# Optimization experiments

Measured on AMD Instinct MI355X. Metric: run time of the kernel, lower is better.

Reference implementation:

```python
import jax, jax.numpy as jnp
import numpy as np
from jax import lax

V, D = 100000, 300          # vocab, embedding dim (pretrained_embeds shape)
F, FS, K = 256, 3, 5        # nof_filters, filters_size, k_for_maxpool
B, NS, LS, LQ = 64, 50, 60, 32  # batch, n_sents per doc, sent len, question len


def setup_inputs() -> dict:
    key = jax.random.key(0)
    ks = jax.random.split(key, 8)
    sentences = jax.random.randint(ks[0], (B, NS, LS), 0, V)
    question = jax.random.randint(ks[1], (B, LQ), 0, V)
    target_sents = jax.random.randint(ks[2], (B, NS), 0, 2)
    target_docs = jax.random.randint(ks[3], (B,), 0, 2)
    embeds = jax.random.normal(ks[4], (V, D), dtype=jnp.float32)          # frozen pretrained table
    filters = jax.random.normal(ks[5], (F, 1, FS, D), dtype=jnp.float32)  # shared quest/sent conv filters
    W = jax.random.normal(ks[6], (6,), dtype=jnp.float32) * 0.4           # linear_per_q weight
    b = jax.random.normal(ks[7], (1,), dtype=jnp.float32) * 0.1           # linear_per_q bias
    return dict(sentences=sentences, question=question, target_sents=target_sents,
                target_docs=target_docs, embeds=embeds, filters=filters, W=W, b=b)


def _conv(x, filters):
    # x: [N,L,D], filters: [F,1,FS,D] -> [N,L,F]; matches F.conv2d(pad=(FS-1,0)) then slicing last L rows
    fs = filters.shape[2]
    L = x.shape[1]
    y = lax.conv_general_dilated(x[:, None, :, :], filters, (1, 1),
                                 ((fs - 1, fs - 1), (0, 0)),
                                 dimension_numbers=('NCHW', 'OIHW', 'NCHW'))  # [N,F,L+fs-1,1]
    return jnp.transpose(y[:, :, -L:, 0], (0, 2, 1))


def _cos(q, s):
    # q: [B,LQ,d], s: [B,NS,LS,d] -> [NS,B,LQ,LS] cosine similarity matrices
    num = jnp.einsum('bqd,bnld->nbql', q, s)
    qn = jnp.linalg.norm(q, axis=-1)                      # [B,LQ]
    sn = jnp.transpose(jnp.linalg.norm(s, axis=-1), (1, 0, 2))  # [NS,B,LS]
    return num / (qn[None, :, :, None] * sn[:, :, None, :])


def _pool(sim, k):
    # k-max pooling over the sentence-length axis -> stack [max, mean-of-top-k]
    top = lax.top_k(sim, k)[0]
    return jnp.stack([top[..., 0], jnp.mean(top, axis=-1)], axis=-1)


def _bce(p, t):
    eps = 1e-7
    p = jnp.clip(p, eps, 1.0 - eps)
    return -jnp.mean(t * jnp.log(p) + (1.0 - t) * jnp.log1p(-p))


def reference(sentences, question, target_sents, target_docs, embeds, filters, W, b):
    qe = embeds[question]                                 # [B,LQ,D]
    se = embeds[sentences]                                # [B,NS,LS,D]
    sim_ins = _cos(qe, se)                                # [NS,B,LQ,LS]
    sim_oh = (sim_ins >= 1.0 - 1e-5).astype(jnp.float32)  # exact-match channel (unmasked, as in original)
    qc = _conv(qe, filters)                               # [B,LQ,F]
    sc = _conv(se.reshape(B * NS, LS, D), filters).reshape(B, NS, LS, F)
    sim_sen = _cos(qc, sc)                                # [NS,B,LQ,LS]
    qmask = (question > 0).astype(jnp.float32)            # pad id = 0
    smask = (sentences > 0).astype(jnp.float32)
    m = qmask[None, :, :, None] * jnp.transpose(smask, (1, 0, 2))[:, :, None, :]
    feats = jnp.concatenate([_pool(sim_ins * m, K), _pool(sim_sen * m, K), _pool(sim_oh, K)], axis=-1)
    feats = jnp.transpose(feats, (1, 0, 2, 3))            # [B,NS,LQ,6]
    sent_out = jax.nn.sigmoid(feats @ W + b[0])           # [B,NS,LQ]
    sentence_relevance = jnp.mean(sent_out, axis=-1)      # [B,NS]
    document_emitions = jnp.max(sentence_relevance, axis=-1)  # [B]
    loss = (_bce(sentence_relevance, target_sents.astype(jnp.float32)) +
            _bce(document_emitions, target_docs.astype(jnp.float32))) / 2.0
    return loss, sentence_relevance, document_emitions
```

## Files before the change

### kernel.cpp

```cpp
#include <hip/hip_runtime.h>
#include <math.h>

#define VB  64
#define NSS 50
#define LSS 60
#define LQQ 32
#define DD  300
#define FF  256

#define SEST 312
#define SROWS 66
#define SCST 264
#define SIMST 66
#define KKC 29
#define KKI 10
#define KKS 8

typedef __attribute__((ext_vector_type(8))) short bfrag;
typedef __attribute__((ext_vector_type(4))) float ffrag;

__device__ __forceinline__ unsigned short f2bf(float v) {
    unsigned int x = __float_as_uint(v);
    x += 0x7fffu + ((x >> 16) & 1u);
    return (unsigned short)(x >> 16);
}
__device__ __forceinline__ float bf2f(unsigned short u) {
    return __uint_as_float(((unsigned int)u) << 16);
}

__global__ __launch_bounds__(256) void k_fprep(const float* __restrict__ filters,
                                               unsigned short* __restrict__ filt_frag) {
    int idx = blockIdx.x * 256 + threadIdx.x;
    const int total = KKC * 16 * 64 * 8;
    if (idx >= total) return;
    int j = idx & 7, ln = (idx >> 3) & 63, nt = (idx >> 9) & 15, kk = idx >> 13;
    int f = nt * 16 + (ln & 15);
    int k = kk * 32 + ((ln >> 4) << 3) + j;
    int t = k / SEST, d = k - t * SEST;
    unsigned short v = 0;
    if (t < 3 && d < DD) v = f2bf(filters[f * 900 + t * DD + d]);
    filt_frag[idx] = v;
}

__global__ __launch_bounds__(512) void k_qprep(const int* __restrict__ question,
                                               const float* __restrict__ embeds,
                                               const unsigned short* __restrict__ filt_frag,
                                               unsigned short* __restrict__ qe_frag,
                                               unsigned short* __restrict__ qc_frag,
                                               float* __restrict__ q_inv,
                                               float* __restrict__ qc_inv) {
    const int b = blockIdx.x, tid = threadIdx.x, lane = tid & 63, w = tid >> 6;
    const int quad = lane >> 4, m16 = lane & 15;
    __shared__ __align__(16) unsigned short qeb[34 * SEST];
    __shared__ __align__(16) unsigned short qcb[LQQ * SCST];
    const int* qrow = question + b * LQQ;
    {
        ushort4 z4 = {0, 0, 0, 0};
        for (int i = tid; i < 96; i += 512) {
            int r = i / 3, c = 300 + (i - r * 3) * 4;
            *(ushort4*)(qeb + r * SEST + c) = z4;
        }
        for (int i = tid; i < 156; i += 512) {
            int r = i / 78, c = (i - r * 78) * 4;
            *(ushort4*)(qeb + (LQQ + r) * SEST + c) = z4;
        }
    }
    for (int i = tid; i < LQQ * 75; i += 512) {
        int r = i / 75, c = (i - r * 75) * 4;
        float4 v = *(const float4*)(embeds + (size_t)qrow[r] * DD + c);
        ushort4 h;
        h.x = f2bf(v.x); h.y = f2bf(v.y); h.z = f2bf(v.z); h.w = f2bf(v.w);
        *(ushort4*)(qeb + r * SEST + c) = h;
    }
    __syncthreads();
    if (tid < 256) {
        int r = tid >> 3, part = tid & 7;
        float s = 0.f;
        #pragma unroll
        for (int it = 0; it < 5; ++it) {
            if (!(it == 4 && part == 7)) {
                int c = part * 8 + it * 64;
                uint4 u = *(const uint4*)(qeb + r * SEST + c);
                float a0 = bf2f((unsigned short)(u.x & 0xffff)), a1 = bf2f((unsigned short)(u.x >> 16));
                float a2 = bf2f((unsigned short)(u.y & 0xffff)), a3 = bf2f((unsigned short)(u.y >> 16));
                float a4 = bf2f((unsigned short)(u.z & 0xffff)), a5 = bf2f((unsigned short)(u.z >> 16));
                float a6 = bf2f((unsigned short)(u.w & 0xffff)), a7 = bf2f((unsigned short)(u.w >> 16));
                s += a0 * a0 + a1 * a1 + a2 * a2 + a3 * a3 + a4 * a4 + a5 * a5 + a6 * a6 + a7 * a7;
            }
        }
        s += __shfl_down(s, 4, 64);
        s += __shfl_down(s, 2, 64);
        s += __shfl_down(s, 1, 64);
        if (part == 0) q_inv[b * LQQ + r] = 1.f / sqrtf(s);
    }
    for (int idx = tid; idx < KKI * 2 * 512; idx += 512) {
        int j = idx & 7, ln = (idx >> 3) & 63, mt = (idx >> 9) & 1, kk = idx >> 10;
        int q = mt * 16 + (ln & 15);
        int k = kk * 32 + ((ln >> 4) << 3) + j;
        qe_frag[(size_t)b * (KKI * 2 * 512) + idx] = (k < DD) ? qeb[q * SEST + k] : (unsigned short)0;
    }
    const int mtq = w & 1, w4 = (w >> 1) * 4;
    ffrag acc[4];
    #pragma unroll
    for (int i = 0; i < 4; ++i) acc[i] = (ffrag)0.f;
    {
        const bfrag* fF = (const bfrag*)filt_frag;
        for (int kk = 0; kk < KKC; ++kk) {
            const int kb = kk * 32 + quad * 8;
            bfrag a0 = *(const bfrag*)(qeb + (mtq * 16 + m16) * SEST + kb);
            bfrag bb[4];
            #pragma unroll
            for (int i = 0; i < 4; ++i) bb[i] = fF[(kk * 16 + w4 + i) * 64 + lane];
            #pragma unroll
            for (int i = 0; i < 4; ++i)
                acc[i] = __builtin_amdgcn_mfma_f32_16x16x32_bf16(a0, bb[i], acc[i], 0, 0, 0);
        }
    }
    #pragma unroll
    for (int i = 0; i < 4; ++i) {
        int f = (w4 + i) * 16 + m16;
        #pragma unroll
        for (int r = 0; r < 4; ++r) {
            int q = mtq * 16 + quad * 4 + r;
            qcb[q * SCST + f] = f2bf(acc[i][r]);
        }
    }
    __syncthreads();
    if (tid < 256) {
        int r = tid >> 3, part = tid & 7;
        float s = 0.f;
        #pragma unroll
        for (int it = 0; it < 4; ++it) {
            int c = part * 8 + it * 64;
            uint4 u = *(const uint4*)(qcb + r * SCST + c);
            float a0 = bf2f((unsigned short)(u.x & 0xffff)), a1 = bf2f((unsigned short)(u.x >> 16));
            float a2 = bf2f((unsigned short)(u.y & 0xffff)), a3 = bf2f((unsigned short)(u.y >> 16));
            float a4 = bf2f((unsigned short)(u.z & 0xffff)), a5 = bf2f((unsigned short)(u.z >> 16));
            float a6 = bf2f((unsigned short)(u.w & 0xffff)), a7 = bf2f((unsigned short)(u.w >> 16));
            s += a0 * a0 + a1 * a1 + a2 * a2 + a3 * a3 + a4 * a4 + a5 * a5 + a6 * a6 + a7 * a7;
        }
        s += __shfl_down(s, 4, 64);
        s += __shfl_down(s, 2, 64);
        s += __shfl_down(s, 1, 64);
        if (part == 0) qc_inv[b * LQQ + r] = 1.f / sqrtf(s);
    }
    for (int idx = tid; idx < KKS * 2 * 512; idx += 512) {
        int j = idx & 7, ln = (idx >> 3) & 63, mt = (idx >> 9) & 1, kk = idx >> 10;
        int q = mt * 16 + (ln & 15);
        int k = kk * 32 + ((ln >> 4) << 3) + j;
        qc_frag[(size_t)b * (KKS * 2 * 512) + idx] = qcb[q * SCST + k];
    }
}

#define CONV_STEP(KKV, BB0, BB1) do {                                              \
    const int kb_ = (KKV) * 32 + quad * 8;                                         \
    bfrag a0_ = *(const bfrag*)(seb + (m16) * SEST + kb_);                         \
    bfrag a1_ = *(const bfrag*)(seb + (16 + m16) * SEST + kb_);                    \
    bfrag a2_ = *(const bfrag*)(seb + (32 + m16) * SEST + kb_);                    \
    bfrag a3_ = *(const bfrag*)(seb + (48 + m16) * SEST + kb_);                    \
    __builtin_amdgcn_s_setprio(1);                                                 \
    acc[0][0] = __builtin_amdgcn_mfma_f32_16x16x32_bf16(a0_, BB0, acc[0][0], 0, 0, 0); \
    acc[0][1] = __builtin_amdgcn_mfma_f32_16x16x32_bf16(a0_, BB1, acc[0][1], 0, 0, 0); \
    acc[1][0] = __builtin_amdgcn_mfma_f32_16x16x32_bf16(a1_, BB0, acc[1][0], 0, 0, 0); \
    acc[1][1] = __builtin_amdgcn_mfma_f32_16x16x32_bf16(a1_, BB1, acc[1][1], 0, 0, 0); \
    acc[2][0] = __builtin_amdgcn_mfma_f32_16x16x32_bf16(a2_, BB0, acc[2][0], 0, 0, 0); \
    acc[2][1] = __builtin_amdgcn_mfma_f32_16x16x32_bf16(a2_, BB1, acc[2][1], 0, 0, 0); \
    acc[3][0] = __builtin_amdgcn_mfma_f32_16x16x32_bf16(a3_, BB0, acc[3][0], 0, 0, 0); \
    acc[3][1] = __builtin_amdgcn_mfma_f32_16x16x32_bf16(a3_, BB1, acc[3][1], 0, 0, 0); \
    __builtin_amdgcn_s_setprio(0);                                                 \
} while (0)

__global__ __launch_bounds__(512, 6) void k_sent(
    const int* __restrict__ sentences, const int* __restrict__ question,
    const float* __restrict__ embeds,
    const unsigned short* __restrict__ filt_frag,
    const unsigned short* __restrict__ qe_frag,
    const unsigned short* __restrict__ qc_frag,
    const float* __restrict__ q_inv, const float* __restrict__ qc_inv,
    const float* __restrict__ W6, const float* __restrict__ b1,
    float* __restrict__ d_out) {
    const int blk = blockIdx.x;
    const int b = blk / NSS, n = blk - b * NSS;
    const int tid = threadIdx.x, lane = tid & 63, w = tid >> 6;
    const int quad = lane >> 4, m16 = lane & 15;
    const int w2 = w * 2;

    __shared__ __align__(16) unsigned short seb[SROWS * SEST];
    __shared__ __align__(16) float sim[LQQ * SIMST];
    __shared__ float sinv[64], scninv[64];
    __shared__ int sid[64];
    __shared__ int qid[LQQ];
    __shared__ float qm[LQQ], qiv[LQQ], qciv[LQQ];
    __shared__ float featq[LQQ][4];
    __shared__ float pr[LQQ];
    unsigned short* scb = seb;

    const bfrag* fF = (const bfrag*)filt_frag;
    bfrag b0a = fF[(w2) * 64 + lane];
    bfrag b0b = fF[(w2 + 1) * 64 + lane];

    const int* srow = sentences + ((size_t)b * NSS + n) * LSS;
    if (tid < 64) sid[tid] = (tid < LSS) ? srow[tid] : 0;
    if (tid < LQQ) {
        int qi = question[b * LQQ + tid];
        qid[tid] = qi; qm[tid] = qi > 0 ? 1.f : 0.f;
        qiv[tid] = q_inv[b * LQQ + tid]; qciv[tid] = qc_inv[b * LQQ + tid];
    }
    {
        ushort4 z4 = {0, 0, 0, 0};
        for (int i = tid; i < 180; i += 512) {
            int r = i / 3, c = 300 + (i - r * 3) * 4;
            *(ushort4*)(seb + r * SEST + c) = z4;
        }
        for (int i = tid; i < 468; i += 512) {
            int r = i / 78, c = (i - r * 78) * 4;
            *(ushort4*)(seb + (60 + r) * SEST + c) = z4;
        }
    }
    for (int i = tid; i < LSS * 75; i += 512) {
        int r = i / 75, c = (i - r * 75) * 4;
        float4 v = *(const float4*)(embeds + (size_t)srow[r] * DD + c);
        ushort4 h;
        h.x = f2bf(v.x); h.y = f2bf(v.y); h.z = f2bf(v.z); h.w = f2bf(v.w);
        *(ushort4*)(seb + r * SEST + c) = h;
    }
    __syncthreads();
    if (tid < 480) {
        int r = tid >> 3, part = tid & 7;
        float s = 0.f;
        #pragma unroll
        for (int it = 0; it < 5; ++it) {
            if (!(it == 4 && part == 7)) {
                int c = part * 8 + it * 64;
                uint4 u = *(const uint4*)(seb + r * SEST + c);
                float a0 = bf2f((unsigned short)(u.x & 0xffff)), a1 = bf2f((unsigned short)(u.x >> 16));
                float a2 = bf2f((unsigned short)(u.y & 0xffff)), a3 = bf2f((unsigned short)(u.y >> 16));
                float a4 = bf2f((unsigned short)(u.z & 0xffff)), a5 = bf2f((unsigned short)(u.z >> 16));
                float a6 = bf2f((unsigned short)(u.w & 0xffff)), a7 = bf2f((unsigned short)(u.w >> 16));
                s += a0 * a0 + a1 * a1 + a2 * a2 + a3 * a3 + a4 * a4 + a5 * a5 + a6 * a6 + a7 * a7;
            }
        }
        s += __shfl_down(s, 4, 64);
        s += __shfl_down(s, 2, 64);
        s += __shfl_down(s, 1, 64);
        if (part == 0) sinv[r] = 1.f / sqrtf(s);
    }
    if (tid >= 480 && tid < 484) sinv[60 + tid - 480] = 0.f;
    __syncthreads();

    ffrag acc[4][2];
    #pragma unroll
    for (int mt = 0; mt < 4; ++mt)
        #pragma unroll
        for (int i = 0; i < 2; ++i) acc[mt][i] = (ffrag)0.f;
    {
        bfrag b1a, b1b;
        for (int kk = 0; kk + 2 <= KKC; kk += 2) {
            b1a = fF[((kk + 1) * 16 + w2) * 64 + lane];
            b1b = fF[((kk + 1) * 16 + w2 + 1) * 64 + lane];
            CONV_STEP(kk, b0a, b0b);
            if (kk + 2 < KKC) {
                b0a = fF[((kk + 2) * 16 + w2) * 64 + lane];
                b0b = fF[((kk + 2) * 16 + w2 + 1) * 64 + lane];
            }
            CONV_STEP(kk + 1, b1a, b1b);
        }
        CONV_STEP(KKC - 1, b0a, b0b);
    }
    {
        const int mt = w >> 2, nt = w & 3;
        const bfrag* qF = (const bfrag*)qe_frag + ((size_t)b * KKI * 2 + mt) * 64 + lane;
        const unsigned short* sebr = seb + (nt * 16 + m16) * SEST + quad * 8;
        ffrag c0 = (ffrag)0.f;
        bfrag aq0 = qF[0];
        for (int kk = 0; kk < KKI; kk += 2) {
            bfrag aq1 = qF[(kk + 1) * 128];
            bfrag bL0 = *(const bfrag*)(sebr + kk * 32);
            c0 = __builtin_amdgcn_mfma_f32_16x16x32_bf16(aq0, bL0, c0, 0, 0, 0);
            if (kk + 2 < KKI) aq0 = qF[(kk + 2) * 128];
            bfrag bL1 = *(const bfrag*)(sebr + (kk + 1) * 32);
            c0 = __builtin_amdgcn_mfma_f32_16x16x32_bf16(aq1, bL1, c0, 0, 0, 0);
        }
        const int l_ = nt * 16 + m16;
        const float sm = sinv[l_] * (sid[l_] > 0 ? 1.f : 0.f);
        #pragma unroll
        for (int r = 0; r < 4; ++r) {
            int q = mt * 16 + quad * 4 + r;
            sim[q * SIMST + l_] = c0[r] * (qiv[q] * qm[q]) * sm;
        }
    }
    __syncthreads();

    if (tid < 256) {
        ushort4 z4 = {0, 0, 0, 0};
        int r4 = 60 + (tid >> 6), c4 = (tid & 63) * 4;
        *(ushort4*)(scb + r4 * SCST + c4) = z4;
    }
    #pragma unroll
    for (int mt = 0; mt < 4; ++mt)
        #pragma unroll
        for (int i = 0; i < 2; ++i) {
            int f = (w2 + i) * 16 + m16;
            #pragma unroll
            for (int r = 0; r < 4; ++r) {
                int l = mt * 16 + quad * 4 + r;
                scb[l * SCST + f] = f2bf(acc[mt][i][r]);
            }
        }
    if (tid < LQQ) {
        int q = tid;
        float t0 = -1e30f, t1 = -1e30f, t2 = -1e30f, t3 = -1e30f, t4 = -1e30f;
        for (int l = 0; l < LSS; ++l) {
            float v = sim[q * SIMST + l];
            if (v > t4) {
                if (v > t0)      { t4 = t3; t3 = t2; t2 = t1; t1 = t0; t0 = v; }
                else if (v > t1) { t4 = t3; t3 = t2; t2 = t1; t1 = v; }
                else if (v > t2) { t4 = t3; t3 = t2; t2 = v; }
                else if (v > t3) { t4 = t3; t3 = v; }
                else               t4 = v;
            }
        }
        featq[q][0] = t0;
        featq[q][1] = (t0 + t1 + t2 + t3 + t4) * 0.2f;
        int qi = qid[q], c = 0;
        for (int l = 0; l < LSS; ++l) c += (sid[l] == qi) ? 1 : 0;
        featq[q][2] = c > 0 ? 1.f : 0.f;
        featq[q][3] = (float)(c < 5 ? c : 5) * 0.2f;
    }
    __syncthreads();
    if (tid < 480) {
        int r = tid >> 3, part = tid & 7;
        float s = 0.f;
        #pragma unroll
        for (int it = 0; it < 4; ++it) {
            int c = part * 8 + it * 64;
            uint4 u = *(const uint4*)(scb + r * SCST + c);
            float a0 = bf2f((unsigned short)(u.x & 0xffff)), a1 = bf2f((unsigned short)(u.x >> 16));
            float a2 = bf2f((unsigned short)(u.y & 0xffff)), a3 = bf2f((unsigned short)(u.y >> 16));
            float a4 = bf2f((unsigned short)(u.z & 0xffff)), a5 = bf2f((unsigned short)(u.z >> 16));
            float a6 = bf2f((unsigned short)(u.w & 0xffff)), a7 = bf2f((unsigned short)(u.w >> 16));
            s += a0 * a0 + a1 * a1 + a2 * a2 + a3 * a3 + a4 * a4 + a5 * a5 + a6 * a6 + a7 * a7;
        }
        s += __shfl_down(s, 4, 64);
        s += __shfl_down(s, 2, 64);
        s += __shfl_down(s, 1, 64);
        if (part == 0) scninv[r] = 1.f / sqrtf(s);
    }
    if (tid >= 480 && tid < 484) scninv[60 + tid - 480] = 0.f;
    __syncthreads();
    {
        const int mt = w >> 2, nt = w & 3;
        const bfrag* qF = (const bfrag*)qc_frag + ((size_t)b * KKS * 2 + mt) * 64 + lane;
        const unsigned short* scbr = scb + (nt * 16 + m16) * SCST + quad * 8;
        ffrag c0 = (ffrag)0.f;
        bfrag aq0 = qF[0];
        for (int kk = 0; kk < KKS; kk += 2) {
            bfrag aq1 = qF[(kk + 1) * 128];
            bfrag bL0 = *(const bfrag*)(scbr + kk * 32);
            c0 = __builtin_amdgcn_mfma_f32_16x16x32_bf16(aq0, bL0, c0, 0, 0, 0);
            if (kk + 2 < KKS) aq0 = qF[(kk + 2) * 128];
            bfrag bL1 = *(const bfrag*)(scbr + (kk + 1) * 32);
            c0 = __builtin_amdgcn_mfma_f32_16x16x32_bf16(aq1, bL1, c0, 0, 0, 0);
        }
        const int l_ = nt * 16 + m16;
        const float sm = scninv[l_] * (sid[l_] > 0 ? 1.f : 0.f);
        #pragma unroll
        for (int r = 0; r < 4; ++r) {
            int q = mt * 16 + quad * 4 + r;
            sim[q * SIMST + l_] = c0[r] * (qciv[q] * qm[q]) * sm;
        }
    }
    __syncthreads();
    if (tid < LQQ) {
        int q = tid;
        float t0 = -1e30f, t1 = -1e30f, t2 = -1e30f, t3 = -1e30f, t4 = -1e30f;
        for (int l = 0; l < LSS; ++l) {
            float v = sim[q * SIMST + l];
            if (v > t4) {
                if (v > t0)      { t4 = t3; t3 = t2; t2 = t1; t1 = t0; t0 = v; }
                else if (v > t1) { t4 = t3; t3 = t2; t2 = t1; t1 = v; }
                else if (v > t2) { t4 = t3; t3 = t2; t2 = v; }
                else if (v > t3) { t4 = t3; t3 = v; }
                else               t4 = v;
            }
        }
        float smax = t0, smean = (t0 + t1 + t2 + t3 + t4) * 0.2f;
        float z = featq[q][0] * W6[0] + featq[q][1] * W6[1] + smax * W6[2] + smean * W6[3]
                + featq[q][2] * W6[4] + featq[q][3] * W6[5] + b1[0];
        pr[q] = 1.f / (1.f + expf(-z));
    }
    __syncthreads();
    if (w == 0) {
        float s = (lane < LQQ) ? pr[lane] : 0.f;
        s += __shfl_down(s, 16, 64);
        s += __shfl_down(s, 8, 64);
        s += __shfl_down(s, 4, 64);
        s += __shfl_down(s, 2, 64);
        s += __shfl_down(s, 1, 64);
        if (lane == 0) d_out[1 + (size_t)b * NSS + n] = s * (1.f / 32.f);
    }
}

__global__ __launch_bounds__(256) void k_final(const int* __restrict__ tsent,
                                               const int* __restrict__ tdoc,
                                               float* __restrict__ d_out) {
    const int tid = threadIdx.x;
    __shared__ float sh[256];
    __shared__ float docs[VB];
    if (tid < VB) {
        float m = -1e30f;
        for (int nn = 0; nn < NSS; ++nn) m = fmaxf(m, d_out[1 + tid * NSS + nn]);
        docs[tid] = m;
        d_out[1 + VB * NSS + tid] = m;
    }
    float s = 0.f;
    for (int i = tid; i < VB * NSS; i += 256) {
        float p = d_out[1 + i];
        p = fminf(fmaxf(p, 1e-7f), 1.f - 1e-7f);
        float t = (float)tsent[i];
        s += t * logf(p) + (1.f - t) * log1pf(-p);
    }
    sh[tid] = s;
    __syncthreads();
    for (int st = 128; st > 0; st >>= 1) {
        if (tid < st) sh[tid] += sh[tid + st];
        __syncthreads();
    }
    float ls = 0.f;
    if (tid == 0) ls = -sh[0] / (float)(VB * NSS);
    __syncthreads();
    float s2 = 0.f;
    if (tid < VB) {
        float p = fminf(fmaxf(docs[tid], 1e-7f), 1.f - 1e-7f);
        float t = (float)tdoc[tid];
        s2 = t * logf(p) + (1.f - t) * log1pf(-p);
    }
    sh[tid] = s2;
    __syncthreads();
    for (int st = 128; st > 0; st >>= 1) {
        if (tid < st) sh[tid] += sh[tid + st];
        __syncthreads();
    }
    if (tid == 0) {
        float ld = -sh[0] / (float)VB;
        d_out[0] = 0.5f * (ls + ld);
    }
}

extern "C" void kernel_launch(void* const* d_in, const int* in_sizes, int n_in,
                              void* d_out, int out_size, void* d_ws, size_t ws_size,
                              hipStream_t stream) {
    const int*   sentences = (const int*)d_in[0];
    const int*   question  = (const int*)d_in[1];
    const int*   tsent     = (const int*)d_in[2];
    const int*   tdoc      = (const int*)d_in[3];
    const float* embeds    = (const float*)d_in[4];
    const float* filters   = (const float*)d_in[5];
    const float* W6        = (const float*)d_in[6];
    const float* b1        = (const float*)d_in[7];
    float* out = (float*)d_out;

    float* ws = (float*)d_ws;
    float* q_inv  = ws;
    float* qc_inv = ws + 2048;
    unsigned short* qe_frag  = (unsigned short*)(ws + 4096);
    unsigned short* qc_frag  = qe_frag + 655360;
    unsigned short* filt_frag = qc_frag + 524288;

    k_fprep<<<928, 256, 0, stream>>>(filters, filt_frag);
    k_qprep<<<VB, 512, 0, stream>>>(question, embeds, filt_frag, qe_frag, qc_frag, q_inv, qc_inv);
    k_sent<<<VB * NSS, 512, 0, stream>>>(sentences, question, embeds,
                                         filt_frag, qe_frag, qc_frag,
                                         q_inv, qc_inv, W6, b1, out);
    k_final<<<1, 256, 0, stream>>>(tsent, tdoc, out);
}
```

Measured before the change: 401.8 us.

## Merge prep kernels, compute norms from registers, deepen filter prefetch in sentence kernel

Folds the filter-fragment prep into the question-prep kernel as extra blocks, with the question conv reading filters directly from global memory. Embedding and conv-output norms are now computed in fp32 straight from loaded values and MFMA accumulators through shuffle reductions, replacing separate passes over bf16 shared memory and removing several block barriers. The sentence-kernel conv loop now prefetches filter fragments three steps ahead instead of two, and the final pooling is collapsed into a single wave. This raises register pressure and computes norms from fp32 values instead of bf16-rounded ones, which slightly changes numerics.

New measurement: 586.4 us. +46.0%, slower.

```diff
diff --git a/kernel.cpp b/kernel.cpp
--- a/kernel.cpp
+++ b/kernel.cpp
@@ -28,31 +28,54 @@
     return __uint_as_float(((unsigned int)u) << 16);
 }
 
-__global__ __launch_bounds__(256) void k_fprep(const float* __restrict__ filters,
-                                               unsigned short* __restrict__ filt_frag) {
-    int idx = blockIdx.x * 256 + threadIdx.x;
-    const int total = KKC * 16 * 64 * 8;
-    if (idx >= total) return;
-    int j = idx & 7, ln = (idx >> 3) & 63, nt = (idx >> 9) & 15, kk = idx >> 13;
-    int f = nt * 16 + (ln & 15);
-    int k = kk * 32 + ((ln >> 4) << 3) + j;
-    int t = k / SEST, d = k - t * SEST;
-    unsigned short v = 0;
-    if (t < 3 && d < DD) v = f2bf(filters[f * 900 + t * DD + d]);
-    filt_frag[idx] = v;
-}
-
-__global__ __launch_bounds__(512) void k_qprep(const int* __restrict__ question,
-                                               const float* __restrict__ embeds,
-                                               const unsigned short* __restrict__ filt_frag,
-                                               unsigned short* __restrict__ qe_frag,
-                                               unsigned short* __restrict__ qc_frag,
-                                               float* __restrict__ q_inv,
-                                               float* __restrict__ qc_inv) {
-    const int b = blockIdx.x, tid = threadIdx.x, lane = tid & 63, w = tid >> 6;
+__device__ __forceinline__ bfrag build_bfrag(const float* __restrict__ filters, int f, int k0) {
+    int t = k0 / SEST, d0 = k0 - t * SEST;
+    union { bfrag b; unsigned short s[8]; } u;
+    if (t < 3 && d0 < DD) {
+        const float* p = filters + f * 900 + t * DD + d0;
+        float4 v0 = *(const float4*)p;
+        u.s[0] = f2bf(v0.x); u.s[1] = f2bf(v0.y); u.s[2] = f2bf(v0.z); u.s[3] = f2bf(v0.w);
+        if (d0 + 4 < DD) {
+            float4 v1 = *(const float4*)(p + 4);
+            u.s[4] = f2bf(v1.x); u.s[5] = f2bf(v1.y); u.s[6] = f2bf(v1.z); u.s[7] = f2bf(v1.w);
+        } else {
+            u.s[4] = 0; u.s[5] = 0; u.s[6] = 0; u.s[7] = 0;
+        }
+    } else {
+        #pragma unroll
+        for (int i = 0; i < 8; ++i) u.s[i] = 0;
+    }
+    return u.b;
+}
+
+__global__ __launch_bounds__(512) void k_prep(const int* __restrict__ question,
+                                              const float* __restrict__ embeds,
+                                              const float* __restrict__ filters,
+                                              unsigned short* __restrict__ filt_frag,
+                                              unsigned short* __restrict__ qe_frag,
+                                              unsigned short* __restrict__ qc_frag,
+                                              float* __restrict__ q_inv,
+                                              float* __restrict__ qc_inv) {
+    const int tid = threadIdx.x;
+    if (blockIdx.x >= VB) {
+        int idx0 = ((blockIdx.x - VB) * 512 + tid) * 4;
+        int j0 = idx0 & 7, ln = (idx0 >> 3) & 63, nt = (idx0 >> 9) & 15, kk = idx0 >> 13;
+        int f = nt * 16 + (ln & 15);
+        int k0 = kk * 32 + ((ln >> 4) << 3) + j0;
+        int t = k0 / SEST, d0 = k0 - t * SEST;
+        ushort4 h = {0, 0, 0, 0};
+        if (t < 3 && d0 < DD) {
+            float4 v = *(const float4*)(filters + f * 900 + t * DD + d0);
+            h.x = f2bf(v.x); h.y = f2bf(v.y); h.z = f2bf(v.z); h.w = f2bf(v.w);
+        }
+        *(ushort4*)(filt_frag + idx0) = h;
+        return;
+    }
+    const int b = blockIdx.x, lane = tid & 63, w = tid >> 6;
     const int quad = lane >> 4, m16 = lane & 15;
     __shared__ __align__(16) unsigned short qeb[34 * SEST];
     __shared__ __align__(16) unsigned short qcb[LQQ * SCST];
+    __shared__ float qpn[LQQ][4];
     const int* qrow = question + b * LQQ;
     {
         ushort4 z4 = {0, 0, 0, 0};
@@ -65,34 +88,24 @@
             *(ushort4*)(qeb + (LQQ + r) * SEST + c) = z4;
         }
     }
-    for (int i = tid; i < LQQ * 75; i += 512) {
-        int r = i / 75, c = (i - r * 75) * 4;
-        float4 v = *(const float4*)(embeds + (size_t)qrow[r] * DD + c);
-        ushort4 h;
-        h.x = f2bf(v.x); h.y = f2bf(v.y); h.z = f2bf(v.z); h.w = f2bf(v.w);
-        *(ushort4*)(qeb + r * SEST + c) = h;
-    }
-    __syncthreads();
-    if (tid < 256) {
-        int r = tid >> 3, part = tid & 7;
+    {
+        const int g = tid >> 4, part = tid & 15;
+        const float* erow = embeds + (size_t)qrow[g] * DD;
         float s = 0.f;
-        #pragma unroll
-        for (int it = 0; it < 5; ++it) {
-            if (!(it == 4 && part == 7)) {
-                int c = part * 8 + it * 64;
-                uint4 u = *(const uint4*)(qeb + r * SEST + c);
-                float a0 = bf2f((unsigned short)(u.x & 0xffff)), a1 = bf2f((unsigned short)(u.x >> 16));
-                float a2 = bf2f((unsigned short)(u.y & 0xffff)), a3 = bf2f((unsigned short)(u.y >> 16));
-                float a4 = bf2f((unsigned short)(u.z & 0xffff)), a5 = bf2f((unsigned short)(u.z >> 16));
-                float a6 = bf2f((unsigned short)(u.w & 0xffff)), a7 = bf2f((unsigned short)(u.w >> 16));
-                s += a0 * a0 + a1 * a1 + a2 * a2 + a3 * a3 + a4 * a4 + a5 * a5 + a6 * a6 + a7 * a7;
-            }
-        }
-        s += __shfl_down(s, 4, 64);
-        s += __shfl_down(s, 2, 64);
-        s += __shfl_down(s, 1, 64);
-        if (part == 0) q_inv[b * LQQ + r] = 1.f / sqrtf(s);
-    }
+        for (int c = part * 4; c < DD; c += 64) {
+            float4 v = *(const float4*)(erow + c);
+            s += v.x * v.x + v.y * v.y + v.z * v.z + v.w * v.w;
+            ushort4 h;
+            h.x = f2bf(v.x); h.y = f2bf(v.y); h.z = f2bf(v.z); h.w = f2bf(v.w);
+            *(ushort4*)(qeb + g * SEST + c) = h;
+        }
+        s += __shfl_down(s, 8, 16);
+        s += __shfl_down(s, 4, 16);
+        s += __shfl_down(s, 2, 16);
+        s += __shfl_down(s, 1, 16);
+        if (part == 0) q_inv[b * LQQ + g] = 1.f / sqrtf(s);
+    }
+    __syncthreads();
     for (int idx = tid; idx < KKI * 2 * 512; idx += 512) {
         int j = idx & 7, ln = (idx >> 3) & 63, mt = (idx >> 9) & 1, kk = idx >> 10;
         int q = mt * 16 + (ln & 15);
@@ -103,18 +116,16 @@
     ffrag acc[4];
     #pragma unroll
     for (int i = 0; i < 4; ++i) acc[i] = (ffrag)0.f;
-    {
-        const bfrag* fF = (const bfrag*)filt_frag;
-        for (int kk = 0; kk < KKC; ++kk) {
-            const int kb = kk * 32 + quad * 8;
-            bfrag a0 = *(const bfrag*)(qeb + (mtq * 16 + m16) * SEST + kb);
-            bfrag bb[4];
-            #pragma unroll
-            for (int i = 0; i < 4; ++i) bb[i] = fF[(kk * 16 + w4 + i) * 64 + lane];
-            #pragma unroll
-            for (int i = 0; i < 4; ++i)
-                acc[i] = __builtin_amdgcn_mfma_f32_16x16x32_bf16(a0, bb[i], acc[i], 0, 0, 0);
-        }
+    for (int kk = 0; kk < KKC; ++kk) {
+        const int kb = kk * 32 + quad * 8;
+        bfrag bb[4];
+        #pragma unroll
+        for (int i = 0; i < 4; ++i)
+            bb[i] = build_bfrag(filters, (w4 + i) * 16 + m16, kb);
+        bfrag a0 = *(const bfrag*)(qeb + (mtq * 16 + m16) * SEST + kb);
+        #pragma unroll
+        for (int i = 0; i < 4; ++i)
+            acc[i] = __builtin_amdgcn_mfma_f32_16x16x32_bf16(a0, bb[i], acc[i], 0, 0, 0);
     }
     #pragma unroll
     for (int i = 0; i < 4; ++i) {
@@ -125,24 +136,20 @@
             qcb[q * SCST + f] = f2bf(acc[i][r]);
         }
     }
-    __syncthreads();
-    if (tid < 256) {
-        int r = tid >> 3, part = tid & 7;
-        float s = 0.f;
-        #pragma unroll
-        for (int it = 0; it < 4; ++it) {
-            int c = part * 8 + it * 64;
-            uint4 u = *(const uint4*)(qcb + r * SCST + c);
-            float a0 = bf2f((unsigned short)(u.x & 0xffff)), a1 = bf2f((unsigned short)(u.x >> 16));
-            float a2 = bf2f((unsigned short)(u.y & 0xffff)), a3 = bf2f((unsigned short)(u.y >> 16));
-            float a4 = bf2f((unsigned short)(u.z & 0xffff)), a5 = bf2f((unsigned short)(u.z >> 16));
-            float a6 = bf2f((unsigned short)(u.w & 0xffff)), a7 = bf2f((unsigned short)(u.w >> 16));
-            s += a0 * a0 + a1 * a1 + a2 * a2 + a3 * a3 + a4 * a4 + a5 * a5 + a6 * a6 + a7 * a7;
-        }
-        s += __shfl_down(s, 4, 64);
-        s += __shfl_down(s, 2, 64);
-        s += __shfl_down(s, 1, 64);
-        if (part == 0) qc_inv[b * LQQ + r] = 1.f / sqrtf(s);
+    #pragma unroll
+    for (int r = 0; r < 4; ++r) {
+        float s = acc[0][r] * acc[0][r] + acc[1][r] * acc[1][r]
+                + acc[2][r] * acc[2][r] + acc[3][r] * acc[3][r];
+        s += __shfl_down(s, 8, 16);
+        s += __shfl_down(s, 4, 16);
+        s += __shfl_down(s, 2, 16);
+        s += __shfl_down(s, 1, 16);
+        if (m16 == 0) qpn[mtq * 16 + quad * 4 + r][w >> 1] = s;
+    }
+    __syncthreads();
+    if (tid < LQQ) {
+        float s = qpn[tid][0] + qpn[tid][1] + qpn[tid][2] + qpn[tid][3];
+        qc_inv[b * LQQ + tid] = 1.f / sqrtf(s);
     }
     for (int idx = tid; idx < KKS * 2 * 512; idx += 512) {
         int j = idx & 7, ln = (idx >> 3) & 63, mt = (idx >> 9) & 1, kk = idx >> 10;
@@ -187,17 +194,17 @@
 
     __shared__ __align__(16) unsigned short seb[SROWS * SEST];
     __shared__ __align__(16) float sim[LQQ * SIMST];
-    __shared__ float sinv[64], scninv[64];
+    __shared__ float sinv[64];
+    __shared__ float pnorm[64][8];
     __shared__ int sid[64];
     __shared__ int qid[LQQ];
     __shared__ float qm[LQQ], qiv[LQQ], qciv[LQQ];
-    __shared__ float featq[LQQ][4];
-    __shared__ float pr[LQQ];
     unsigned short* scb = seb;
 
     const bfrag* fF = (const bfrag*)filt_frag;
-    bfrag b0a = fF[(w2) * 64 + lane];
-    bfrag b0b = fF[(w2 + 1) * 64 + lane];
+    bfrag pa0 = fF[(0 * 16 + w2) * 64 + lane], pb0 = fF[(0 * 16 + w2 + 1) * 64 + lane];
+    bfrag pa1 = fF[(1 * 16 + w2) * 64 + lane], pb1 = fF[(1 * 16 + w2 + 1) * 64 + lane];
+    bfrag pa2 = fF[(2 * 16 + w2) * 64 + lane], pb2 = fF[(2 * 16 + w2 + 1) * 64 + lane];
 
     const int* srow = sentences + ((size_t)b * NSS + n) * LSS;
     if (tid < 64) sid[tid] = (tid < LSS) ? srow[tid] : 0;
@@ -217,35 +224,26 @@
             *(ushort4*)(seb + (60 + r) * SEST + c) = z4;
         }
     }
-    for (int i = tid; i < LSS * 75; i += 512) {
-        int r = i / 75, c = (i - r * 75) * 4;
-        float4 v = *(const float4*)(embeds + (size_t)srow[r] * DD + c);
-        ushort4 h;
-        h.x = f2bf(v.x); h.y = f2bf(v.y); h.z = f2bf(v.z); h.w = f2bf(v.w);
-        *(ushort4*)(seb + r * SEST + c) = h;
-    }
-    __syncthreads();
-    if (tid < 480) {
-        int r = tid >> 3, part = tid & 7;
-        float s = 0.f;
-        #pragma unroll
-        for (int it = 0; it < 5; ++it) {
-            if (!(it == 4 && part == 7)) {
-                int c = part * 8 + it * 64;
-                uint4 u = *(const uint4*)(seb + r * SEST + c);
-                float a0 = bf2f((unsigned short)(u.x & 0xffff)), a1 = bf2f((unsigned short)(u.x >> 16));
-                float a2 = bf2f((unsigned short)(u.y & 0xffff)), a3 = bf2f((unsigned short)(u.y >> 16));
-                float a4 = bf2f((unsigned short)(u.z & 0xffff)), a5 = bf2f((unsigned short)(u.z >> 16));
-                float a6 = bf2f((unsigned short)(u.w & 0xffff)), a7 = bf2f((unsigned short)(u.w >> 16));
-                s += a0 * a0 + a1 * a1 + a2 * a2 + a3 * a3 + a4 * a4 + a5 * a5 + a6 * a6 + a7 * a7;
+    {
+        const int g = tid >> 3, part = tid & 7;
+        if (g < LSS) {
+            const float* erow = embeds + (size_t)srow[g] * DD;
+            float s = 0.f;
+            for (int c = part * 4; c < DD; c += 32) {
+                float4 v = *(const float4*)(erow + c);
+                s += v.x * v.x + v.y * v.y + v.z * v.z + v.w * v.w;
+                ushort4 h;
+                h.x = f2bf(v.x); h.y = f2bf(v.y); h.z = f2bf(v.z); h.w = f2bf(v.w);
+                *(ushort4*)(seb + g * SEST + c) = h;
             }
-        }
-        s += __shfl_down(s, 4, 64);
-        s += __shfl_down(s, 2, 64);
-        s += __shfl_down(s, 1, 64);
-        if (part == 0) sinv[r] = 1.f / sqrtf(s);
-    }
-    if (tid >= 480 && tid < 484) sinv[60 + tid - 480] = 0.f;
+            s += __shfl_down(s, 4, 8);
+            s += __shfl_down(s, 2, 8);
+            s += __shfl_down(s, 1, 8);
+            if (part == 0) sinv[g] = 1.f / sqrtf(s);
+        } else if (part == 0) {
+            sinv[g] = 0.f;
+        }
+    }
     __syncthreads();
 
     ffrag acc[4][2];
@@ -254,18 +252,25 @@
         #pragma unroll
         for (int i = 0; i < 2; ++i) acc[mt][i] = (ffrag)0.f;
     {
-        bfrag b1a, b1b;
-        for (int kk = 0; kk + 2 <= KKC; kk += 2) {
-            b1a = fF[((kk + 1) * 16 + w2) * 64 + lane];
-            b1b = fF[((kk + 1) * 16 + w2 + 1) * 64 + lane];
-            CONV_STEP(kk, b0a, b0b);
-            if (kk + 2 < KKC) {
-                b0a = fF[((kk + 2) * 16 + w2) * 64 + lane];
-                b0b = fF[((kk + 2) * 16 + w2 + 1) * 64 + lane];
-            }
-            CONV_STEP(kk + 1, b1a, b1b);
-        }
-        CONV_STEP(KKC - 1, b0a, b0b);
+        for (int kk = 0; kk < 24; kk += 3) {
+            bfrag na0 = fF[((kk + 3) * 16 + w2) * 64 + lane];
+            bfrag nb0 = fF[((kk + 3) * 16 + w2 + 1) * 64 + lane];
+            CONV_STEP(kk, pa0, pb0);
+            bfrag na1 = fF[((kk + 4) * 16 + w2) * 64 + lane];
+            bfrag nb1 = fF[((kk + 4) * 16 + w2 + 1) * 64 + lane];
+            CONV_STEP(kk + 1, pa1, pb1);
+            bfrag na2 = fF[((kk + 5) * 16 + w2) * 64 + lane];
+            bfrag nb2 = fF[((kk + 5) * 16 + w2 + 1) * 64 + lane];
+            CONV_STEP(kk + 2, pa2, pb2);
+            pa0 = na0; pb0 = nb0; pa1 = na1; pb1 = nb1; pa2 = na2; pb2 = nb2;
+        }
+        bfrag ta = fF[(27 * 16 + w2) * 64 + lane], tb = fF[(27 * 16 + w2 + 1) * 64 + lane];
+        bfrag ua = fF[(28 * 16 + w2) * 64 + lane], ub = fF[(28 * 16 + w2 + 1) * 64 + lane];
+        CONV_STEP(24, pa0, pb0);
+        CONV_STEP(25, pa1, pb1);
+        CONV_STEP(26, pa2, pb2);
+        CONV_STEP(27, ta, tb);
+        CONV_STEP(28, ua, ub);
     }
     {
         const int mt = w >> 2, nt = w & 3;
@@ -291,6 +296,7 @@
     }
     __syncthreads();
 
+    float fq0 = 0.f, fq1 = 0.f, fq2 = 0.f, fq3 = 0.f;
     if (tid < 256) {
         ushort4 z4 = {0, 0, 0, 0};
         int r4 = 60 + (tid >> 6), c4 = (tid & 63) * 4;
@@ -306,6 +312,17 @@
                 int l = mt * 16 + quad * 4 + r;
                 scb[l * SCST + f] = f2bf(acc[mt][i][r]);
             }
+        }
+    #pragma unroll
+    for (int mt = 0; mt < 4; ++mt)
+        #pragma unroll
+        for (int r = 0; r < 4; ++r) {
+            float s = acc[mt][0][r] * acc[mt][0][r] + acc[mt][1][r] * acc[mt][1][r];
+            s += __shfl_down(s, 8, 16);
+            s += __shfl_down(s, 4, 16);
+            s += __shfl_down(s, 2, 16);
+            s += __shfl_down(s, 1, 16);
+            if (m16 == 0) pnorm[mt * 16 + quad * 4 + r][w] = s;
         }
     if (tid < LQQ) {
         int q = tid;
@@ -320,34 +337,15 @@
                 else               t4 = v;
             }
         }
-        featq[q][0] = t0;
-        featq[q][1] = (t0 + t1 + t2 + t3 + t4) * 0.2f;
+        fq0 = t0;
+        fq1 = (t0 + t1 + t2 + t3 + t4) * 0.2f;
         int qi = qid[q], c = 0;
         for (int l = 0; l < LSS; ++l) c += (sid[l] == qi) ? 1 : 0;
-        featq[q][2] = c > 0 ? 1.f : 0.f;
-        featq[q][3] = (float)(c < 5 ? c : 5) * 0.2f;
-    }
-    __syncthreads();
-    if (tid < 480) {
-        int r = tid >> 3, part = tid & 7;
-        float s = 0.f;
-        #pragma unroll
-        for (int it = 0; it < 4; ++it) {
-            int c = part * 8 + it * 64;
-            uint4 u = *(const uint4*)(scb + r * SCST + c);
-            float a0 = bf2f((unsigned short)(u.x & 0xffff)), a1 = bf2f((unsigned short)(u.x >> 16));
-            float a2 = bf2f((unsigned short)(u.y & 0xffff)), a3 = bf2f((unsigned short)(u.y >> 16));
-            float a4 = bf2f((unsigned short)(u.z & 0xffff)), a5 = bf2f((unsigned short)(u.z >> 16));
-            float a6 = bf2f((unsigned short)(u.w & 0xffff)), a7 = bf2f((unsigned short)(u.w >> 16));
-            s += a0 * a0 + a1 * a1 + a2 * a2 + a3 * a3 + a4 * a4 + a5 * a5 + a6 * a6 + a7 * a7;
-        }
-        s += __shfl_down(s, 4, 64);
-        s += __shfl_down(s, 2, 64);
-        s += __shfl_down(s, 1, 64);
-        if (part == 0) scninv[r] = 1.f / sqrtf(s);
-    }
-    if (tid >= 480 && tid < 484) scninv[60 + tid - 480] = 0.f;
-    __syncthreads();
+        fq2 = c > 0 ? 1.f : 0.f;
+        fq3 = (float)(c < 5 ? c : 5) * 0.2f;
+    }
+    __syncthreads();
+
     {
         const int mt = w >> 2, nt = w & 3;
         const bfrag* qF = (const bfrag*)qc_frag + ((size_t)b * KKS * 2 + mt) * 64 + lane;
@@ -363,7 +361,10 @@
             c0 = __builtin_amdgcn_mfma_f32_16x16x32_bf16(aq1, bL1, c0, 0, 0, 0);
         }
         const int l_ = nt * 16 + m16;
-        const float sm = scninv[l_] * (sid[l_] > 0 ? 1.f : 0.f);
+        float ssum = 0.f;
+        #pragma unroll
+        for (int t = 0; t < 8; ++t) ssum += pnorm[l_][t];
+        const float sm = (1.f / sqrtf(ssum)) * (sid[l_] > 0 ? 1.f : 0.f);
         #pragma unroll
         for (int r = 0; r < 4; ++r) {
             int q = mt * 16 + quad * 4 + r;
@@ -371,33 +372,33 @@
         }
     }
     __syncthreads();
-    if (tid < LQQ) {
-        int q = tid;
-        float t0 = -1e30f, t1 = -1e30f, t2 = -1e30f, t3 = -1e30f, t4 = -1e30f;
-        for (int l = 0; l < LSS; ++l) {
-            float v = sim[q * SIMST + l];
-            if (v > t4) {
-                if (v > t0)      { t4 = t3; t3 = t2; t2 = t1; t1 = t0; t0 = v; }
-                else if (v > t1) { t4 = t3; t3 = t2; t2 = t1; t1 = v; }
-                else if (v > t2) { t4 = t3; t3 = t2; t2 = v; }
-                else if (v > t3) { t4 = t3; t3 = v; }
-                else               t4 = v;
+
+    if (w == 0) {
+        float prv = 0.f;
+        if (lane < LQQ) {
+            int q = lane;
+            float t0 = -1e30f, t1 = -1e30f, t2 = -1e30f, t3 = -1e30f, t4 = -1e30f;
+            for (int l = 0; l < LSS; ++l) {
+                float v = sim[q * SIMST + l];
+                if (v > t4) {
+                    if (v > t0)      { t4 = t3; t3 = t2; t2 = t1; t1 = t0; t0 = v; }
+                    else if (v > t1) { t4 = t3; t3 = t2; t2 = t1; t1 = v; }
+                    else if (v > t2) { t4 = t3; t3 = t2; t2 = v; }
+                    else if (v > t3) { t4 = t3; t3 = v; }
+                    else               t4 = v;
+                }
             }
-        }
-        float smax = t0, smean = (t0 + t1 + t2 + t3 + t4) * 0.2f;
-        float z = featq[q][0] * W6[0] + featq[q][1] * W6[1] + smax * W6[2] + smean * W6[3]
-                + featq[q][2] * W6[4] + featq[q][3] * W6[5] + b1[0];
-        pr[q] = 1.f / (1.f + expf(-z));
-    }
-    __syncthreads();
-    if (w == 0) {
-        float s = (lane < LQQ) ? pr[lane] : 0.f;
-        s += __shfl_down(s, 16, 64);
-        s += __shfl_down(s, 8, 64);
-        s += __shfl_down(s, 4, 64);
-        s += __shfl_down(s, 2, 64);
-        s += __shfl_down(s, 1, 64);
-        if (lane == 0) d_out[1 + (size_t)b * NSS + n] = s * (1.f / 32.f);
+            float smax = t0, smean = (t0 + t1 + t2 + t3 + t4) * 0.2f;
+            float z = fq0 * W6[0] + fq1 * W6[1] + smax * W6[2] + smean * W6[3]
+                    + fq2 * W6[4] + fq3 * W6[5] + b1[0];
+            prv = 1.f / (1.f + expf(-z));
+        }
+        prv += __shfl_down(prv, 16, 64);
+        prv += __shfl_down(prv, 8, 64);
+        prv += __shfl_down(prv, 4, 64);
+        prv += __shfl_down(prv, 2, 64);
+        prv += __shfl_down(prv, 1, 64);
+        if (lane == 0) d_out[1 + (size_t)b * NSS + n] = prv * (1.f / 32.f);
     }
 }
 
@@ -467,8 +468,8 @@
     unsigned short* qc_frag  = qe_frag + 655360;
     unsigned short* filt_frag = qc_frag + 524288;
 
-    k_fprep<<<928, 256, 0, stream>>>(filters, filt_frag);
-    k_qprep<<<VB, 512, 0, stream>>>(question, embeds, filt_frag, qe_frag, qc_frag, q_inv, qc_inv);
+    k_prep<<<VB + 116, 512, 0, stream>>>(question, embeds, filters,
+                                         filt_frag, qe_frag, qc_frag, q_inv, qc_inv);
     k_sent<<<VB * NSS, 512, 0, stream>>>(sentences, question, embeds,
                                          filt_frag, qe_frag, qc_frag,
                                          q_inv, qc_inv, W6, b1, out);
```

## Fuse final loss into sentence kernel via last-block counter; vectorize prep kernels

Applied to the files above, without the earlier changes.

Removes the separate single-block loss kernel. The last k_sent block to finish, detected with an atomic counter, now computes the document max and both BCE terms. The filter and question fragment-prep loops now use 4- and 8-element vector loads and stores instead of scalar ones. The question conv loop also prefetches the next filter fragments into registers before running the MFMAs. This saves one launch and some prep time, at the cost of an atomic and fence in every k_sent block and a serial tail done by one wave.

After: 509.5 us. +26.8%, slower.

```diff
diff --git a/kernel.cpp b/kernel.cpp
--- a/kernel.cpp
+++ b/kernel.cpp
@@ -29,17 +29,20 @@
 }
 
 __global__ __launch_bounds__(256) void k_fprep(const float* __restrict__ filters,
-                                               unsigned short* __restrict__ filt_frag) {
-    int idx = blockIdx.x * 256 + threadIdx.x;
-    const int total = KKC * 16 * 64 * 8;
-    if (idx >= total) return;
-    int j = idx & 7, ln = (idx >> 3) & 63, nt = (idx >> 9) & 15, kk = idx >> 13;
+                                               unsigned short* __restrict__ filt_frag,
+                                               int* __restrict__ ctr) {
+    if (blockIdx.x == 0 && threadIdx.x == 0) *ctr = 0;
+    int idx0 = (blockIdx.x * 256 + threadIdx.x) * 4;
+    int j0 = idx0 & 7, ln = (idx0 >> 3) & 63, nt = (idx0 >> 9) & 15, kk = idx0 >> 13;
     int f = nt * 16 + (ln & 15);
-    int k = kk * 32 + ((ln >> 4) << 3) + j;
-    int t = k / SEST, d = k - t * SEST;
-    unsigned short v = 0;
-    if (t < 3 && d < DD) v = f2bf(filters[f * 900 + t * DD + d]);
-    filt_frag[idx] = v;
+    int k0 = kk * 32 + ((ln >> 4) << 3) + j0;
+    int t = k0 / SEST, d0 = k0 - t * SEST;
+    ushort4 h = {0, 0, 0, 0};
+    if (t < 3 && d0 < DD) {
+        float4 v = *(const float4*)(filters + f * 900 + t * DD + d0);
+        h.x = f2bf(v.x); h.y = f2bf(v.y); h.z = f2bf(v.z); h.w = f2bf(v.w);
+    }
+    *(ushort4*)(filt_frag + idx0) = h;
 }
 
 __global__ __launch_bounds__(512) void k_qprep(const int* __restrict__ question,
@@ -93,11 +96,13 @@
         s += __shfl_down(s, 1, 64);
         if (part == 0) q_inv[b * LQQ + r] = 1.f / sqrtf(s);
     }
-    for (int idx = tid; idx < KKI * 2 * 512; idx += 512) {
-        int j = idx & 7, ln = (idx >> 3) & 63, mt = (idx >> 9) & 1, kk = idx >> 10;
+    for (int i8 = tid; i8 < KKI * 2 * 64; i8 += 512) {
+        int ln = i8 & 63, mt = (i8 >> 6) & 1, kk = i8 >> 7;
         int q = mt * 16 + (ln & 15);
-        int k = kk * 32 + ((ln >> 4) << 3) + j;
-        qe_frag[(size_t)b * (KKI * 2 * 512) + idx] = (k < DD) ? qeb[q * SEST + k] : (unsigned short)0;
+        int k0 = kk * 32 + ((ln >> 4) << 3);
+        uint4 v = {0, 0, 0, 0};
+        if (k0 < SEST) v = *(const uint4*)(qeb + q * SEST + k0);
+        *(uint4*)(qe_frag + (size_t)b * (KKI * 2 * 512) + (size_t)i8 * 8) = v;
     }
     const int mtq = w & 1, w4 = (w >> 1) * 4;
     ffrag acc[4];
@@ -105,15 +110,21 @@
     for (int i = 0; i < 4; ++i) acc[i] = (ffrag)0.f;
     {
         const bfrag* fF = (const bfrag*)filt_frag;
+        bfrag bb[4], nb[4];
+        #pragma unroll
+        for (int i = 0; i < 4; ++i) bb[i] = fF[(w4 + i) * 64 + lane];
         for (int kk = 0; kk < KKC; ++kk) {
+            if (kk + 1 < KKC) {
+                #pragma unroll
+                for (int i = 0; i < 4; ++i) nb[i] = fF[((kk + 1) * 16 + w4 + i) * 64 + lane];
+            }
             const int kb = kk * 32 + quad * 8;
             bfrag a0 = *(const bfrag*)(qeb + (mtq * 16 + m16) * SEST + kb);
-            bfrag bb[4];
-            #pragma unroll
-            for (int i = 0; i < 4; ++i) bb[i] = fF[(kk * 16 + w4 + i) * 64 + lane];
             #pragma unroll
             for (int i = 0; i < 4; ++i)
                 acc[i] = __builtin_amdgcn_mfma_f32_16x16x32_bf16(a0, bb[i], acc[i], 0, 0, 0);
+            #pragma unroll
+            for (int i = 0; i < 4; ++i) bb[i] = nb[i];
         }
     }
     #pragma unroll
@@ -144,11 +155,12 @@
         s += __shfl_down(s, 1, 64);
         if (part == 0) qc_inv[b * LQQ + r] = 1.f / sqrtf(s);
     }
-    for (int idx = tid; idx < KKS * 2 * 512; idx += 512) {
-        int j = idx & 7, ln = (idx >> 3) & 63, mt = (idx >> 9) & 1, kk = idx >> 10;
+    for (int i8 = tid; i8 < KKS * 2 * 64; i8 += 512) {
+        int ln = i8 & 63, mt = (i8 >> 6) & 1, kk = i8 >> 7;
         int q = mt * 16 + (ln & 15);
-        int k = kk * 32 + ((ln >> 4) << 3) + j;
-        qc_frag[(size_t)b * (KKS * 2 * 512) + idx] = qcb[q * SCST + k];
+        int k0 = kk * 32 + ((ln >> 4) << 3);
+        *(uint4*)(qc_frag + (size_t)b * (KKS * 2 * 512) + (size_t)i8 * 8) =
+            *(const uint4*)(qcb + q * SCST + k0);
     }
 }
 
@@ -178,6 +190,8 @@
     const unsigned short* __restrict__ qc_frag,
     const float* __restrict__ q_inv, const float* __restrict__ qc_inv,
     const float* __restrict__ W6, const float* __restrict__ b1,
+    const int* __restrict__ tsent, const int* __restrict__ tdoc,
+    int* __restrict__ ctr,
     float* __restrict__ d_out) {
     const int blk = blockIdx.x;
     const int b = blk / NSS, n = blk - b * NSS;
@@ -398,52 +412,43 @@
         s += __shfl_down(s, 2, 64);
         s += __shfl_down(s, 1, 64);
         if (lane == 0) d_out[1 + (size_t)b * NSS + n] = s * (1.f / 32.f);
-    }
-}
-
-__global__ __launch_bounds__(256) void k_final(const int* __restrict__ tsent,
-                                               const int* __restrict__ tdoc,
-                                               float* __restrict__ d_out) {
-    const int tid = threadIdx.x;
-    __shared__ float sh[256];
-    __shared__ float docs[VB];
-    if (tid < VB) {
-        float m = -1e30f;
-        for (int nn = 0; nn < NSS; ++nn) m = fmaxf(m, d_out[1 + tid * NSS + nn]);
-        docs[tid] = m;
-        d_out[1 + VB * NSS + tid] = m;
-    }
-    float s = 0.f;
-    for (int i = tid; i < VB * NSS; i += 256) {
-        float p = d_out[1 + i];
-        p = fminf(fmaxf(p, 1e-7f), 1.f - 1e-7f);
-        float t = (float)tsent[i];
-        s += t * logf(p) + (1.f - t) * log1pf(-p);
-    }
-    sh[tid] = s;
-    __syncthreads();
-    for (int st = 128; st > 0; st >>= 1) {
-        if (tid < st) sh[tid] += sh[tid + st];
-        __syncthreads();
-    }
-    float ls = 0.f;
-    if (tid == 0) ls = -sh[0] / (float)(VB * NSS);
-    __syncthreads();
-    float s2 = 0.f;
-    if (tid < VB) {
-        float p = fminf(fmaxf(docs[tid], 1e-7f), 1.f - 1e-7f);
-        float t = (float)tdoc[tid];
-        s2 = t * logf(p) + (1.f - t) * log1pf(-p);
-    }
-    sh[tid] = s2;
-    __syncthreads();
-    for (int st = 128; st > 0; st >>= 1) {
-        if (tid < st) sh[tid] += sh[tid + st];
-        __syncthreads();
-    }
-    if (tid == 0) {
-        float ld = -sh[0] / (float)VB;
-        d_out[0] = 0.5f * (ls + ld);
+
+        int last = 0;
+        if (lane == 0) {
+            __threadfence();
+            int old = __hip_atomic_fetch_add(ctr, 1, __ATOMIC_ACQ_REL, __HIP_MEMORY_SCOPE_AGENT);
+            last = (old == VB * NSS - 1) ? 1 : 0;
+        }
+        last = __shfl(last, 0, 64);
+        if (last) {
+            float m = -1e30f;
+            for (int nn = 0; nn < NSS; ++nn) {
+                float v = __hip_atomic_load(d_out + 1 + lane * NSS + nn,
+                                            __ATOMIC_RELAXED, __HIP_MEMORY_SCOPE_AGENT);
+                m = fmaxf(m, v);
+            }
+            d_out[1 + VB * NSS + lane] = m;
+            float ssent = 0.f;
+            for (int i = lane; i < VB * NSS; i += 64) {
+                float p = __hip_atomic_load(d_out + 1 + i,
+                                            __ATOMIC_RELAXED, __HIP_MEMORY_SCOPE_AGENT);
+                p = fminf(fmaxf(p, 1e-7f), 1.f - 1e-7f);
+                float t = (float)tsent[i];
+                ssent += t * logf(p) + (1.f - t) * log1pf(-p);
+            }
+            #pragma unroll
+            for (int off = 32; off > 0; off >>= 1) ssent += __shfl_down(ssent, off, 64);
+            float p2 = fminf(fmaxf(m, 1e-7f), 1.f - 1e-7f);
+            float t2 = (float)tdoc[lane];
+            float sdoc = t2 * logf(p2) + (1.f - t2) * log1pf(-p2);
+            #pragma unroll
+            for (int off = 32; off > 0; off >>= 1) sdoc += __shfl_down(sdoc, off, 64);
+            if (lane == 0) {
+                float ls = -ssent / (float)(VB * NSS);
+                float ld = -sdoc / (float)VB;
+                d_out[0] = 0.5f * (ls + ld);
+            }
+        }
     }
 }
 
@@ -466,11 +471,12 @@
     unsigned short* qe_frag  = (unsigned short*)(ws + 4096);
     unsigned short* qc_frag  = qe_frag + 655360;
     unsigned short* filt_frag = qc_frag + 524288;
-
-    k_fprep<<<928, 256, 0, stream>>>(filters, filt_frag);
+    int* ctr = (int*)(filt_frag + 237568);
+
+    k_fprep<<<232, 256, 0, stream>>>(filters, filt_frag, ctr);
     k_qprep<<<VB, 512, 0, stream>>>(question, embeds, filt_frag, qe_frag, qc_frag, q_inv, qc_inv);
     k_sent<<<VB * NSS, 512, 0, stream>>>(sentences, question, embeds,
                                          filt_frag, qe_frag, qc_frag,
-                                         q_inv, qc_inv, W6, b1, out);
-    k_final<<<1, 256, 0, stream>>>(tsent, tdoc, out);
-}
+                                         q_inv, qc_inv, W6, b1,
+                                         tsent, tdoc, ctr, out);
+}
```
